# Optimization experiments

Hardware: AMD Instinct MI355X
Metric: run time of the kernel (lower is better)

## Reference

```python
import jax, jax.numpy as jnp
import numpy as np

B, T, D, E, TOP_K = 8, 2048, 512, 8, 2


def setup_inputs() -> dict:
    key = jax.random.key(0)
    ks = jax.random.split(key, 8)
    s = 0.02
    return {
        "x": jax.random.normal(ks[0], (B, T, D), dtype=jnp.float32),
        "eps": jax.random.normal(ks[1], (B, T, E), dtype=jnp.float32),
        "Wr": jax.random.normal(ks[2], (D, E), dtype=jnp.float32) * s,
        "br": jnp.zeros((E,), dtype=jnp.float32),
        "Wn": jax.random.normal(ks[3], (D, E), dtype=jnp.float32) * s,
        "bn": jnp.zeros((E,), dtype=jnp.float32),
        "Wk": jax.random.normal(ks[4], (E, D, D), dtype=jnp.float32) * s,
        "bk": jnp.zeros((E, D), dtype=jnp.float32),
    }


def reference(x, eps, Wr, br, Wn, bn, Wk, bk):
    # Noisy top-k router (NoisyTopkRouter.forward)
    logits = jnp.einsum("btd,de->bte", x, Wr) + br            # [B,T,E]
    noise_logits = jnp.einsum("btd,de->bte", x, Wn) + bn      # [B,T,E]
    noisy = logits + eps * jax.nn.softplus(noise_logits)      # [B,T,E]
    _, top_idx = jax.lax.top_k(noisy, TOP_K)                  # [B,T,k]
    # mask[b,t,e] = True iff expert e is in the token's top-k
    topk_mask = jax.nn.one_hot(top_idx, E, dtype=jnp.float32).sum(-2) > 0
    sparse_logits = jnp.where(topk_mask, noisy, -jnp.inf)
    gating = jax.nn.softmax(sparse_logits, axis=-1)           # zero for non-top-k experts
    # Dense dispatch: every expert's Linear applied to all tokens, then
    # gating (zero outside top-k) selects/scales — same math as the masked
    # gather + per-expert Linear + gating scale in SparseMoE.forward.
    expert_out = jnp.einsum("btd,edh->bteh", x, Wk) + bk      # [B,T,E,D]
    out = jnp.einsum("bte,bteh->bth", gating, expert_out)     # [B,T,D]
    return out
```

## Files before the change

kernel.cpp:

```cpp
#include <hip/hip_runtime.h>
#include <hip/hip_bf16.h>
#include <math.h>

#define B_    8
#define T_    2048
#define NTOK  (B_ * T_)
#define D_    512
#define E_    8
#define NPAIR 28
#define CAP   NTOK

#define WL_MAX 160

#define RV_TOK    16
#define RV_THR    256
#define XS_STRIDE 132
#define WS_FLOATS 2108

typedef __attribute__((ext_vector_type(4))) float f32x4;
typedef __attribute__((ext_vector_type(8))) short short8;

__device__ __forceinline__ void async_load16(const void* g, void* l) {
    __builtin_amdgcn_global_load_lds(
        (const __attribute__((address_space(1))) unsigned int*)g,
        (__attribute__((address_space(3))) unsigned int*)l,
        16, 0, 0);
}

__global__ __launch_bounds__(256) void transpose_wk(
    const float* __restrict__ Wk, __hip_bfloat16* __restrict__ Wkt)
{
    __shared__ float tile[32][33];
    const int e  = blockIdx.z;
    const int d0 = blockIdx.x * 32;
    const int h0 = blockIdx.y * 32;
    const int tx = threadIdx.x, ty = threadIdx.y;

    const float* src = Wk + ((size_t)e * D_ + d0) * D_ + h0;
    #pragma unroll
    for (int r = ty; r < 32; r += 8)
        tile[r][tx] = src[(size_t)r * D_ + tx];
    __syncthreads();
    __hip_bfloat16* dst = Wkt + ((size_t)e * D_ + h0) * D_ + d0;
    #pragma unroll
    for (int r = ty; r < 32; r += 8)
        dst[(size_t)r * D_ + tx] = __float2bfloat16(tile[tx][r]);
}

__global__ __launch_bounds__(RV_THR) void router_kernel(
    const float* __restrict__ x,
    const float* __restrict__ eps,
    const float* __restrict__ Wr,
    const float* __restrict__ br,
    const float* __restrict__ Wn,
    const float* __restrict__ bn,
    __hip_bfloat16* __restrict__ xb,
    uint4* __restrict__ top2)
{
    __shared__ float xs[RV_TOK * XS_STRIDE];
    __shared__ float wsh[WS_FLOATS];

    const int tid  = threadIdx.x;
    const int tok0 = blockIdx.x * RV_TOK;
    const int lane = tid & 63, wv = tid >> 6;
    const int kidx = lane >> 2, ts = lane & 3;
    const int tl = wv * 4 + ts;
    const int wk = tid >> 1, wh = tid & 1;

    float acc[16];
    #pragma unroll
    for (int c = 0; c < 16; ++c) acc[c] = 0.f;

    for (int kc = 0; kc < D_; kc += 128) {
        #pragma unroll
        for (int it = 0; it < 2; ++it) {
            const int f   = it * RV_THR + tid;
            const int row = f >> 5, col = (f & 31) * 4;
            const f32x4 v = *(const f32x4*)(x + (size_t)(tok0 + row) * D_ + kc + col);
            *(f32x4*)(xs + row * XS_STRIDE + col) = v;
            union { __hip_bfloat16 h[4]; uint2 u; } cv;
            cv.h[0] = __float2bfloat16(v.x); cv.h[1] = __float2bfloat16(v.y);
            cv.h[2] = __float2bfloat16(v.z); cv.h[3] = __float2bfloat16(v.w);
            *(uint2*)(xb + (size_t)(tok0 + row) * D_ + kc + col) = cv.u;
        }
        {
            const float* src = (wh ? Wn : Wr) + (size_t)(kc + wk) * E_;
            const f32x4 w0 = *(const f32x4*)(src);
            const f32x4 w1 = *(const f32x4*)(src + 4);
            float* dst = wsh + wk * 16 + (wk >> 3) * 4 + wh * 8;
            *(f32x4*)(dst)     = w0;
            *(f32x4*)(dst + 4) = w1;
        }
        __syncthreads();

        const float* xra = xs + tl * XS_STRIDE + kidx * 8;
        const f32x4 xa0 = *(const f32x4*)(xra);
        const f32x4 xa1 = *(const f32x4*)(xra + 4);
        const float* wbase = wsh + kidx * 132;
        #pragma unroll
        for (int kk = 0; kk < 8; ++kk) {
            const float xav = (kk < 4) ? xa0[kk] : xa1[kk - 4];
            const float* wrow = wbase + kk * 16;
            #pragma unroll
            for (int c4 = 0; c4 < 4; ++c4) {
                const f32x4 w = *(const f32x4*)(wrow + c4 * 4);
                #pragma unroll
                for (int c = 0; c < 4; ++c)
                    acc[c4 * 4 + c] = fmaf(xav, w[c], acc[c4 * 4 + c]);
            }
        }
        __syncthreads();
    }

    #pragma unroll
    for (int off = 4; off < 64; off <<= 1) {
        #pragma unroll
        for (int c = 0; c < 16; ++c)
            acc[c] += __shfl_xor(acc[c], off);
    }

    if (lane < 4) {
        const int tok = tok0 + tl;
        float nv[8];
        #pragma unroll
        for (int e = 0; e < 8; ++e) {
            const float nl = acc[8 + e] + bn[e];
            const float sp = fmaxf(nl, 0.f) + log1pf(expf(-fabsf(nl)));
            nv[e] = acc[e] + br[e] + eps[(size_t)tok * E_ + e] * sp;
        }
        int i1 = 0; float v1 = nv[0];
        #pragma unroll
        for (int e = 1; e < 8; ++e)
            if (nv[e] > v1) { v1 = nv[e]; i1 = e; }
        int i2 = -1; float v2 = -3.4e38f;
        #pragma unroll
        for (int e = 0; e < 8; ++e)
            if (e != i1 && nv[e] > v2) { v2 = nv[e]; i2 = e; }
        const float t  = expf(v2 - v1);
        const float g1 = 1.f / (1.f + t);
        const float g2 = t / (1.f + t);
        top2[tok] = make_uint4((unsigned)i1 | ((unsigned)i2 << 8),
                               __float_as_uint(g1), __float_as_uint(g2), 0u);
    }
}

__global__ __launch_bounds__(256) void bucket_kernel(
    const uint4* __restrict__ top2,
    int* __restrict__ counts,
    uint4* __restrict__ entries)
{
    __shared__ int hist[NPAIR];
    __shared__ int base[NPAIR];
    const int tid = threadIdx.x;
    const int tok = blockIdx.x * 256 + tid;
    if (tid < NPAIR) hist[tid] = 0;
    __syncthreads();
    const uint4 t = top2[tok];
    const int i1 = t.x & 0xff, i2 = (t.x >> 8) & 0xff;
    const int a = min(i1, i2), b = max(i1, i2);
    const unsigned ga = (i1 < i2) ? t.y : t.z;
    const unsigned gb = (i1 < i2) ? t.z : t.y;
    const int p = a * (15 - a) / 2 + (b - a - 1);
    const int l = atomicAdd(&hist[p], 1);
    __syncthreads();
    if (tid < NPAIR) base[tid] = atomicAdd(counts + tid, hist[tid]);
    __syncthreads();
    entries[(size_t)p * CAP + base[p] + l] = make_uint4((unsigned)tok, ga, gb, 0u);
}

__global__ __launch_bounds__(64) void build_wl(
    const int* __restrict__ counts, int* __restrict__ wl)
{
    const int t = threadIdx.x;
    const int nm = (t < NPAIR) ? ((counts[t] + 127) >> 7) : 0;
    int inc = nm;
    #pragma unroll
    for (int d = 1; d < 64; d <<= 1) {
        const int v = __shfl_up(inc, d);
        if (t >= d) inc += v;
    }
    if (t == 63) wl[0] = inc;
    const int ex = inc - nm;
    for (int m = 0; m < nm; ++m)
        wl[1 + ex + m] = (t << 8) | m;
}

__global__ __launch_bounds__(256, 2) void moe_gemm(
    const __hip_bfloat16* __restrict__ xb,
    const __hip_bfloat16* __restrict__ wkt,
    const float* __restrict__ bk,
    const int* __restrict__ counts,
    const uint4* __restrict__ entries,
    const int* __restrict__ wl,
    float* __restrict__ out)
{
    constexpr int BM = 128, BN = 128, BK = 32;
    constexpr int NT = D_ / BK;
    __shared__ __hip_bfloat16 As[3][BM * BK];
    __shared__ __hip_bfloat16 Bs[3][2][BN * BK];
    __shared__ uint4 ent[BM];

    const int id = blockIdx.x;
    const int g = id >> 5, r = id & 31;
    const int nt = r >> 3;
    const int mi = g * 8 + (r & 7);
    const int nmtot = wl[0];
    if (mi >= nmtot) return;
    const int we = wl[1 + mi];
    const int p = we >> 8, mt = we & 255;
    const int cnt = counts[p];

    int e1 = 0, rem = p;
    while (rem >= 7 - e1) { rem -= 7 - e1; ++e1; }
    const int e2 = e1 + 1 + rem;

    const int tid = threadIdx.x;
    const int wave = tid >> 6, lane = tid & 63;

    if (tid < BM) {
        const int idx = mt * BM + tid;
        ent[tid] = (idx < cnt) ? entries[(size_t)p * CAP + idx]
                               : make_uint4(0u, 0u, 0u, 0u);
    }
    __syncthreads();

    const int quad = lane >> 4, lr = lane & 15;
    const int wm = wave >> 1, wn = wave & 1;

    const int r16 = lane >> 2;
    const int csel = (lane & 3) ^ ((lane >> 3) & 3);
    const int rA0 = wave * 32 + r16;
    const size_t tA0 = ent[rA0].x;
    const size_t tA1 = ent[rA0 + 16].x;
    const __hip_bfloat16* gA0 = xb + tA0 * D_ + csel * 8;
    const __hip_bfloat16* gA1 = xb + tA1 * D_ + csel * 8;
    const __hip_bfloat16* gB1 = wkt + ((size_t)e1 * D_ + nt * BN + rA0) * D_ + csel * 8;
    const __hip_bfloat16* gB2 = wkt + ((size_t)e2 * D_ + nt * BN + rA0) * D_ + csel * 8;

    const int so = (quad ^ ((lr >> 1) & 3)) * 8;

    f32x4 accA[4][4], accB[4][4];
    #pragma unroll
    for (int i = 0; i < 4; ++i)
        #pragma unroll
        for (int j = 0; j < 4; ++j) {
            accA[i][j] = (f32x4){0.f, 0.f, 0.f, 0.f};
            accB[i][j] = (f32x4){0.f, 0.f, 0.f, 0.f};
        }

#define STAGE(buf, k0) do {                                        \
        __hip_bfloat16* aB  = &As[buf][wave * 1024];               \
        __hip_bfloat16* b1B = &Bs[buf][0][wave * 1024];            \
        __hip_bfloat16* b2B = &Bs[buf][1][wave * 1024];            \
        async_load16(gA0 + (k0), aB);                              \
        async_load16(gA1 + (k0), aB + 512);                        \
        async_load16(gB1 + (k0), b1B);                             \
        async_load16(gB1 + 16 * D_ + (k0), b1B + 512);             \
        async_load16(gB2 + (k0), b2B);                             \
        async_load16(gB2 + 16 * D_ + (k0), b2B + 512);             \
    } while (0)

#define COMPUTE(buf) do {                                                      \
        short8 a[4], b1v[4], b2v[4];                                           \
        _Pragma("unroll")                                                      \
        for (int i = 0; i < 4; ++i)                                            \
            a[i] = *(const short8*)(&As[buf][(wm * 64 + i * 16 + lr) * 32 + so]); \
        _Pragma("unroll")                                                      \
        for (int j = 0; j < 4; ++j) {                                          \
            b1v[j] = *(const short8*)(&Bs[buf][0][(wn * 64 + j * 16 + lr) * 32 + so]); \
            b2v[j] = *(const short8*)(&Bs[buf][1][(wn * 64 + j * 16 + lr) * 32 + so]); \
        }                                                                      \
        __builtin_amdgcn_s_setprio(1);                                         \
        _Pragma("unroll")                                                      \
        for (int i = 0; i < 4; ++i)                                            \
            _Pragma("unroll")                                                  \
            for (int j = 0; j < 4; ++j) {                                      \
                accA[i][j] = __builtin_amdgcn_mfma_f32_16x16x32_bf16(          \
                    a[i], b1v[j], accA[i][j], 0, 0, 0);                        \
                accB[i][j] = __builtin_amdgcn_mfma_f32_16x16x32_bf16(          \
                    a[i], b2v[j], accB[i][j], 0, 0, 0);                        \
            }                                                                  \
        __builtin_amdgcn_s_setprio(0);                                         \
    } while (0)

    STAGE(0, 0);
    STAGE(1, BK);

    #pragma unroll
    for (int t = 0; t < NT - 1; ++t) {
        asm volatile("s_waitcnt vmcnt(6)" ::: "memory");
        __builtin_amdgcn_s_barrier();
        if (t + 2 < NT) STAGE((t + 2) % 3, (t + 2) * BK);
        COMPUTE(t % 3);
    }
    asm volatile("s_waitcnt vmcnt(0)" ::: "memory");
    __builtin_amdgcn_s_barrier();
    COMPUTE((NT - 1) % 3);

#undef STAGE
#undef COMPUTE

    const int colbase = nt * BN + wn * 64 + lr;
    float bkA[4], bkB[4];
    #pragma unroll
    for (int j = 0; j < 4; ++j) {
        bkA[j] = bk[e1 * D_ + colbase + j * 16];
        bkB[j] = bk[e2 * D_ + colbase + j * 16];
    }

    #pragma unroll
    for (int i = 0; i < 4; ++i) {
        #pragma unroll
        for (int rr = 0; rr < 4; ++rr) {
            const int row = wm * 64 + i * 16 + quad * 4 + rr;
            if (mt * BM + row < cnt) {
                const uint4 en = ent[row];
                const float ga = __uint_as_float(en.y);
                const float gb = __uint_as_float(en.z);
                float* orow = out + (size_t)en.x * D_ + colbase;
                #pragma unroll
                for (int j = 0; j < 4; ++j)
                    orow[j * 16] = ga * (accA[i][j][rr] + bkA[j])
                                 + gb * (accB[i][j][rr] + bkB[j]);
            }
        }
    }
}

extern "C" void kernel_launch(void* const* d_in, const int* in_sizes, int n_in,
                              void* d_out, int out_size, void* d_ws, size_t ws_size,
                              hipStream_t stream) {
    const float* x   = (const float*)d_in[0];
    const float* eps = (const float*)d_in[1];
    const float* Wr  = (const float*)d_in[2];
    const float* br  = (const float*)d_in[3];
    const float* Wn  = (const float*)d_in[4];
    const float* bn  = (const float*)d_in[5];
    const float* Wk  = (const float*)d_in[6];
    const float* bk  = (const float*)d_in[7];
    float* out = (float*)d_out;

    char* ws = (char*)d_ws;
    size_t off = 0;
    int* counts = (int*)(ws + off);                     off += 256;
    uint4* entries = (uint4*)(ws + off);                off += (size_t)NPAIR * CAP * 16;
    __hip_bfloat16* xb = (__hip_bfloat16*)(ws + off);   off += (size_t)NTOK * D_ * 2;
    __hip_bfloat16* wkt = (__hip_bfloat16*)(ws + off);  off += (size_t)E_ * D_ * D_ * 2;
    uint4* top2 = (uint4*)(ws + off);                   off += (size_t)NTOK * 16;
    int* wl = (int*)(ws + off);                         off += 1024;
    (void)ws_size;

    hipMemsetAsync(counts, 0, NPAIR * sizeof(int), stream);

    transpose_wk<<<dim3(16, 16, E_), dim3(32, 8), 0, stream>>>(Wk, wkt);
    router_kernel<<<dim3(NTOK / RV_TOK), dim3(RV_THR), 0, stream>>>(
        x, eps, Wr, br, Wn, bn, xb, top2);
    bucket_kernel<<<dim3(NTOK / 256), dim3(256), 0, stream>>>(top2, counts, entries);
    build_wl<<<dim3(1), dim3(64), 0, stream>>>(counts, wl);
    moe_gemm<<<dim3(WL_MAX * 4), dim3(256), 0, stream>>>(
        xb, wkt, bk, counts, entries, wl, out);
}
```

Baseline: 162.5 us.

## Fuse router, transpose, bucketing and worklist into one prep kernel; double-buffer GEMM

Merges the Wk transpose, router, bucket and worklist-build kernels into a single launch. Router blocks append entries with global atomics, and the last finishing block builds the worklist, so the top2 buffer and three launches go away. The GEMM drops from a 3-stage to a 2-stage LDS pipeline with an extra barrier per k-step, to reach 3 blocks per CU. This trades pipeline depth for occupancy, and global atomics on 28 counters may contend.

```diff
diff --git a/kernel.cpp b/kernel.cpp
--- a/kernel.cpp
+++ b/kernel.cpp
@@ -17,6 +17,10 @@
 #define XS_STRIDE 132
 #define WS_FLOATS 2108
 
+#define PREP_ROUTER_BLOCKS (NTOK / RV_TOK)
+#define PREP_TRANS_BLOCKS  (16 * 16 * E_)
+#define PREP_BLOCKS (PREP_ROUTER_BLOCKS + PREP_TRANS_BLOCKS)
+
 typedef __attribute__((ext_vector_type(4))) float f32x4;
 typedef __attribute__((ext_vector_type(8))) short short8;
 
@@ -27,165 +31,159 @@
         16, 0, 0);
 }
 
-__global__ __launch_bounds__(256) void transpose_wk(
-    const float* __restrict__ Wk, __hip_bfloat16* __restrict__ Wkt)
-{
-    __shared__ float tile[32][33];
-    const int e  = blockIdx.z;
-    const int d0 = blockIdx.x * 32;
-    const int h0 = blockIdx.y * 32;
-    const int tx = threadIdx.x, ty = threadIdx.y;
-
-    const float* src = Wk + ((size_t)e * D_ + d0) * D_ + h0;
-    #pragma unroll
-    for (int r = ty; r < 32; r += 8)
-        tile[r][tx] = src[(size_t)r * D_ + tx];
-    __syncthreads();
-    __hip_bfloat16* dst = Wkt + ((size_t)e * D_ + h0) * D_ + d0;
-    #pragma unroll
-    for (int r = ty; r < 32; r += 8)
-        dst[(size_t)r * D_ + tx] = __float2bfloat16(tile[tx][r]);
-}
-
-__global__ __launch_bounds__(RV_THR) void router_kernel(
+__global__ __launch_bounds__(256) void prep_kernel(
     const float* __restrict__ x,
     const float* __restrict__ eps,
     const float* __restrict__ Wr,
     const float* __restrict__ br,
     const float* __restrict__ Wn,
     const float* __restrict__ bn,
+    const float* __restrict__ Wk,
     __hip_bfloat16* __restrict__ xb,
-    uint4* __restrict__ top2)
+    __hip_bfloat16* __restrict__ wkt,
+    int* __restrict__ counts,
+    uint4* __restrict__ entries,
+    int* __restrict__ done,
+    int* __restrict__ wl)
 {
-    __shared__ float xs[RV_TOK * XS_STRIDE];
-    __shared__ float wsh[WS_FLOATS];
-
-    const int tid  = threadIdx.x;
-    const int tok0 = blockIdx.x * RV_TOK;
-    const int lane = tid & 63, wv = tid >> 6;
-    const int kidx = lane >> 2, ts = lane & 3;
-    const int tl = wv * 4 + ts;
-    const int wk = tid >> 1, wh = tid & 1;
-
-    float acc[16];
-    #pragma unroll
-    for (int c = 0; c < 16; ++c) acc[c] = 0.f;
-
-    for (int kc = 0; kc < D_; kc += 128) {
-        #pragma unroll
-        for (int it = 0; it < 2; ++it) {
-            const int f   = it * RV_THR + tid;
-            const int row = f >> 5, col = (f & 31) * 4;
-            const f32x4 v = *(const f32x4*)(x + (size_t)(tok0 + row) * D_ + kc + col);
-            *(f32x4*)(xs + row * XS_STRIDE + col) = v;
-            union { __hip_bfloat16 h[4]; uint2 u; } cv;
-            cv.h[0] = __float2bfloat16(v.x); cv.h[1] = __float2bfloat16(v.y);
-            cv.h[2] = __float2bfloat16(v.z); cv.h[3] = __float2bfloat16(v.w);
-            *(uint2*)(xb + (size_t)(tok0 + row) * D_ + kc + col) = cv.u;
-        }
-        {
-            const float* src = (wh ? Wn : Wr) + (size_t)(kc + wk) * E_;
-            const f32x4 w0 = *(const f32x4*)(src);
-            const f32x4 w1 = *(const f32x4*)(src + 4);
-            float* dst = wsh + wk * 16 + (wk >> 3) * 4 + wh * 8;
-            *(f32x4*)(dst)     = w0;
-            *(f32x4*)(dst + 4) = w1;
-        }
+    __shared__ float smem[RV_TOK * XS_STRIDE + WS_FLOATS];
+    __shared__ int lastBlock;
+    const int bid = blockIdx.x, tid = threadIdx.x;
+
+    if (bid < PREP_ROUTER_BLOCKS) {
+        float* xs  = smem;
+        float* wsh = smem + RV_TOK * XS_STRIDE;
+
+        const int tok0 = bid * RV_TOK;
+        const int lane = tid & 63, wv = tid >> 6;
+        const int kidx = lane >> 2, ts = lane & 3;
+        const int tl = wv * 4 + ts;
+        const int wk = tid >> 1, wh = tid & 1;
+
+        float acc[16];
+        #pragma unroll
+        for (int c = 0; c < 16; ++c) acc[c] = 0.f;
+
+        for (int kc = 0; kc < D_; kc += 128) {
+            #pragma unroll
+            for (int it = 0; it < 2; ++it) {
+                const int f   = it * RV_THR + tid;
+                const int row = f >> 5, col = (f & 31) * 4;
+                const f32x4 v = *(const f32x4*)(x + (size_t)(tok0 + row) * D_ + kc + col);
+                *(f32x4*)(xs + row * XS_STRIDE + col) = v;
+                union { __hip_bfloat16 h[4]; uint2 u; } cv;
+                cv.h[0] = __float2bfloat16(v.x); cv.h[1] = __float2bfloat16(v.y);
+                cv.h[2] = __float2bfloat16(v.z); cv.h[3] = __float2bfloat16(v.w);
+                *(uint2*)(xb + (size_t)(tok0 + row) * D_ + kc + col) = cv.u;
+            }
+            {
+                const float* src = (wh ? Wn : Wr) + (size_t)(kc + wk) * E_;
+                const f32x4 w0 = *(const f32x4*)(src);
+                const f32x4 w1 = *(const f32x4*)(src + 4);
+                float* dst = wsh + wk * 16 + (wk >> 3) * 4 + wh * 8;
+                *(f32x4*)(dst)     = w0;
+                *(f32x4*)(dst + 4) = w1;
+            }
+            __syncthreads();
+
+            const float* xra = xs + tl * XS_STRIDE + kidx * 8;
+            const f32x4 xa0 = *(const f32x4*)(xra);
+            const f32x4 xa1 = *(const f32x4*)(xra + 4);
+            const float* wbase = wsh + kidx * 132;
+            #pragma unroll
+            for (int kk = 0; kk < 8; ++kk) {
+                const float xav = (kk < 4) ? xa0[kk] : xa1[kk - 4];
+                const float* wrow = wbase + kk * 16;
+                #pragma unroll
+                for (int c4 = 0; c4 < 4; ++c4) {
+                    const f32x4 w = *(const f32x4*)(wrow + c4 * 4);
+                    #pragma unroll
+                    for (int c = 0; c < 4; ++c)
+                        acc[c4 * 4 + c] = fmaf(xav, w[c], acc[c4 * 4 + c]);
+                }
+            }
+            __syncthreads();
+        }
+
+        #pragma unroll
+        for (int off = 4; off < 64; off <<= 1) {
+            #pragma unroll
+            for (int c = 0; c < 16; ++c)
+                acc[c] += __shfl_xor(acc[c], off);
+        }
+
+        if (lane < 4) {
+            const int tok = tok0 + tl;
+            float nv[8];
+            #pragma unroll
+            for (int e = 0; e < 8; ++e) {
+                const float nl = acc[8 + e] + bn[e];
+                const float sp = fmaxf(nl, 0.f) + log1pf(expf(-fabsf(nl)));
+                nv[e] = acc[e] + br[e] + eps[(size_t)tok * E_ + e] * sp;
+            }
+            int i1 = 0; float v1 = nv[0];
+            #pragma unroll
+            for (int e = 1; e < 8; ++e)
+                if (nv[e] > v1) { v1 = nv[e]; i1 = e; }
+            int i2 = -1; float v2 = -3.4e38f;
+            #pragma unroll
+            for (int e = 0; e < 8; ++e)
+                if (e != i1 && nv[e] > v2) { v2 = nv[e]; i2 = e; }
+            const float t  = expf(v2 - v1);
+            const float g1 = 1.f / (1.f + t);
+            const float g2 = t / (1.f + t);
+            const int aa = min(i1, i2), bb = max(i1, i2);
+            const float gae = (i1 < i2) ? g1 : g2;
+            const float gbe = (i1 < i2) ? g2 : g1;
+            const int p = aa * (15 - aa) / 2 + (bb - aa - 1);
+            const int slot = atomicAdd(&counts[p], 1);
+            entries[(size_t)p * CAP + slot] =
+                make_uint4((unsigned)tok, __float_as_uint(gae),
+                           __float_as_uint(gbe), 0u);
+        }
+    } else {
+        const int idx = bid - PREP_ROUTER_BLOCKS;
+        const int e  = idx >> 8;
+        const int rem = idx & 255;
+        const int d0 = (rem & 15) * 32;
+        const int h0 = (rem >> 4) * 32;
+        const int tx = tid & 31, ty = tid >> 5;
+        float (*tile)[33] = reinterpret_cast<float(*)[33]>(smem);
+
+        const float* src = Wk + ((size_t)e * D_ + d0) * D_ + h0;
+        #pragma unroll
+        for (int r = ty; r < 32; r += 8)
+            tile[r][tx] = src[(size_t)r * D_ + tx];
         __syncthreads();
-
-        const float* xra = xs + tl * XS_STRIDE + kidx * 8;
-        const f32x4 xa0 = *(const f32x4*)(xra);
-        const f32x4 xa1 = *(const f32x4*)(xra + 4);
-        const float* wbase = wsh + kidx * 132;
-        #pragma unroll
-        for (int kk = 0; kk < 8; ++kk) {
-            const float xav = (kk < 4) ? xa0[kk] : xa1[kk - 4];
-            const float* wrow = wbase + kk * 16;
-            #pragma unroll
-            for (int c4 = 0; c4 < 4; ++c4) {
-                const f32x4 w = *(const f32x4*)(wrow + c4 * 4);
-                #pragma unroll
-                for (int c = 0; c < 4; ++c)
-                    acc[c4 * 4 + c] = fmaf(xav, w[c], acc[c4 * 4 + c]);
-            }
-        }
-        __syncthreads();
-    }
-
-    #pragma unroll
-    for (int off = 4; off < 64; off <<= 1) {
-        #pragma unroll
-        for (int c = 0; c < 16; ++c)
-            acc[c] += __shfl_xor(acc[c], off);
-    }
-
-    if (lane < 4) {
-        const int tok = tok0 + tl;
-        float nv[8];
-        #pragma unroll
-        for (int e = 0; e < 8; ++e) {
-            const float nl = acc[8 + e] + bn[e];
-            const float sp = fmaxf(nl, 0.f) + log1pf(expf(-fabsf(nl)));
-            nv[e] = acc[e] + br[e] + eps[(size_t)tok * E_ + e] * sp;
-        }
-        int i1 = 0; float v1 = nv[0];
-        #pragma unroll
-        for (int e = 1; e < 8; ++e)
-            if (nv[e] > v1) { v1 = nv[e]; i1 = e; }
-        int i2 = -1; float v2 = -3.4e38f;
-        #pragma unroll
-        for (int e = 0; e < 8; ++e)
-            if (e != i1 && nv[e] > v2) { v2 = nv[e]; i2 = e; }
-        const float t  = expf(v2 - v1);
-        const float g1 = 1.f / (1.f + t);
-        const float g2 = t / (1.f + t);
-        top2[tok] = make_uint4((unsigned)i1 | ((unsigned)i2 << 8),
-                               __float_as_uint(g1), __float_as_uint(g2), 0u);
+        __hip_bfloat16* dst = wkt + ((size_t)e * D_ + h0) * D_ + d0;
+        #pragma unroll
+        for (int r = ty; r < 32; r += 8)
+            dst[(size_t)r * D_ + tx] = __float2bfloat16(tile[tx][r]);
+    }
+
+    __threadfence();
+    __syncthreads();
+    if (tid == 0)
+        lastBlock = (atomicAdd(done, 1) == PREP_BLOCKS - 1) ? 1 : 0;
+    __syncthreads();
+    if (lastBlock && tid < 64) {
+        const int t = tid;
+        const int c = (t < NPAIR) ? atomicAdd(&counts[t], 0) : 0;
+        const int nm = (c + 127) >> 7;
+        int inc = nm;
+        #pragma unroll
+        for (int d = 1; d < 64; d <<= 1) {
+            const int v = __shfl_up(inc, d);
+            if (t >= d) inc += v;
+        }
+        if (t == 63) wl[0] = inc;
+        const int ex = inc - nm;
+        for (int m = 0; m < nm; ++m)
+            wl[1 + ex + m] = (t << 8) | m;
     }
 }
 
-__global__ __launch_bounds__(256) void bucket_kernel(
-    const uint4* __restrict__ top2,
-    int* __restrict__ counts,
-    uint4* __restrict__ entries)
-{
-    __shared__ int hist[NPAIR];
-    __shared__ int base[NPAIR];
-    const int tid = threadIdx.x;
-    const int tok = blockIdx.x * 256 + tid;
-    if (tid < NPAIR) hist[tid] = 0;
-    __syncthreads();
-    const uint4 t = top2[tok];
-    const int i1 = t.x & 0xff, i2 = (t.x >> 8) & 0xff;
-    const int a = min(i1, i2), b = max(i1, i2);
-    const unsigned ga = (i1 < i2) ? t.y : t.z;
-    const unsigned gb = (i1 < i2) ? t.z : t.y;
-    const int p = a * (15 - a) / 2 + (b - a - 1);
-    const int l = atomicAdd(&hist[p], 1);
-    __syncthreads();
-    if (tid < NPAIR) base[tid] = atomicAdd(counts + tid, hist[tid]);
-    __syncthreads();
-    entries[(size_t)p * CAP + base[p] + l] = make_uint4((unsigned)tok, ga, gb, 0u);
-}
-
-__global__ __launch_bounds__(64) void build_wl(
-    const int* __restrict__ counts, int* __restrict__ wl)
-{
-    const int t = threadIdx.x;
-    const int nm = (t < NPAIR) ? ((counts[t] + 127) >> 7) : 0;
-    int inc = nm;
-    #pragma unroll
-    for (int d = 1; d < 64; d <<= 1) {
-        const int v = __shfl_up(inc, d);
-        if (t >= d) inc += v;
-    }
-    if (t == 63) wl[0] = inc;
-    const int ex = inc - nm;
-    for (int m = 0; m < nm; ++m)
-        wl[1 + ex + m] = (t << 8) | m;
-}
-
-__global__ __launch_bounds__(256, 2) void moe_gemm(
+__global__ __launch_bounds__(256, 3) void moe_gemm(
     const __hip_bfloat16* __restrict__ xb,
     const __hip_bfloat16* __restrict__ wkt,
     const float* __restrict__ bk,
@@ -196,8 +194,8 @@
 {
     constexpr int BM = 128, BN = 128, BK = 32;
     constexpr int NT = D_ / BK;
-    __shared__ __hip_bfloat16 As[3][BM * BK];
-    __shared__ __hip_bfloat16 Bs[3][2][BN * BK];
+    __shared__ __hip_bfloat16 As[2][BM * BK];
+    __shared__ __hip_bfloat16 Bs[2][2][BN * BK];
     __shared__ uint4 ent[BM];
 
     const int id = blockIdx.x;
@@ -260,8 +258,7 @@
         async_load16(gB2 + 16 * D_ + (k0), b2B + 512);             \
     } while (0)
 
-#define COMPUTE(buf) do {                                                      \
-        short8 a[4], b1v[4], b2v[4];                                           \
+#define READS(buf) do {                                                        \
         _Pragma("unroll")                                                      \
         for (int i = 0; i < 4; ++i)                                            \
             a[i] = *(const short8*)(&As[buf][(wm * 64 + i * 16 + lr) * 32 + so]); \
@@ -270,6 +267,9 @@
             b1v[j] = *(const short8*)(&Bs[buf][0][(wn * 64 + j * 16 + lr) * 32 + so]); \
             b2v[j] = *(const short8*)(&Bs[buf][1][(wn * 64 + j * 16 + lr) * 32 + so]); \
         }                                                                      \
+    } while (0)
+
+#define MFMAS() do {                                                           \
         __builtin_amdgcn_s_setprio(1);                                         \
         _Pragma("unroll")                                                      \
         for (int i = 0; i < 4; ++i)                                            \
@@ -286,19 +286,27 @@
     STAGE(0, 0);
     STAGE(1, BK);
 
-    #pragma unroll
     for (int t = 0; t < NT - 1; ++t) {
+        short8 a[4], b1v[4], b2v[4];
         asm volatile("s_waitcnt vmcnt(6)" ::: "memory");
         __builtin_amdgcn_s_barrier();
-        if (t + 2 < NT) STAGE((t + 2) % 3, (t + 2) * BK);
-        COMPUTE(t % 3);
-    }
-    asm volatile("s_waitcnt vmcnt(0)" ::: "memory");
-    __builtin_amdgcn_s_barrier();
-    COMPUTE((NT - 1) % 3);
+        READS(t & 1);
+        asm volatile("s_waitcnt lgkmcnt(0)" ::: "memory");
+        __builtin_amdgcn_s_barrier();
+        if (t + 2 < NT) STAGE(t & 1, (t + 2) * BK);
+        MFMAS();
+    }
+    {
+        short8 a[4], b1v[4], b2v[4];
+        asm volatile("s_waitcnt vmcnt(0)" ::: "memory");
+        __builtin_amdgcn_s_barrier();
+        READS((NT - 1) & 1);
+        MFMAS();
+    }
 
 #undef STAGE
-#undef COMPUTE
+#undef READS
+#undef MFMAS
 
     const int colbase = nt * BN + wn * 64 + lr;
     float bkA[4], bkB[4];
@@ -346,17 +354,14 @@
     uint4* entries = (uint4*)(ws + off);                off += (size_t)NPAIR * CAP * 16;
     __hip_bfloat16* xb = (__hip_bfloat16*)(ws + off);   off += (size_t)NTOK * D_ * 2;
     __hip_bfloat16* wkt = (__hip_bfloat16*)(ws + off);  off += (size_t)E_ * D_ * D_ * 2;
-    uint4* top2 = (uint4*)(ws + off);                   off += (size_t)NTOK * 16;
     int* wl = (int*)(ws + off);                         off += 1024;
+    int* done = counts + 32;
     (void)ws_size;
 
-    hipMemsetAsync(counts, 0, NPAIR * sizeof(int), stream);
-
-    transpose_wk<<<dim3(16, 16, E_), dim3(32, 8), 0, stream>>>(Wk, wkt);
-    router_kernel<<<dim3(NTOK / RV_TOK), dim3(RV_THR), 0, stream>>>(
-        x, eps, Wr, br, Wn, bn, xb, top2);
-    bucket_kernel<<<dim3(NTOK / 256), dim3(256), 0, stream>>>(top2, counts, entries);
-    build_wl<<<dim3(1), dim3(64), 0, stream>>>(counts, wl);
+    hipMemsetAsync(counts, 0, 256, stream);
+
+    prep_kernel<<<dim3(PREP_BLOCKS), dim3(256), 0, stream>>>(
+        x, eps, Wr, br, Wn, bn, Wk, xb, wkt, counts, entries, done, wl);
     moe_gemm<<<dim3(WL_MAX * 4), dim3(256), 0, stream>>>(
         xb, wkt, bk, counts, entries, wl, out);
 }
```

Result: slower. 475.4 us (+192.6%).
